# Kernel tuning notes

Measured on AMD Instinct MI355X. Metric: run time of the kernel, lower is better.

Reference implementation:

```python
import jax, jax.numpy as jnp
import numpy as np

N, C, H = 4096, 1024, 16
HD = C // H            # 64
DR = HD // 8           # 8 rope freqs per spatial axis


def setup_inputs() -> dict:
    key = jax.random.key(0)
    k1, k2, k3, k4, k5, k6 = jax.random.split(key, 6)
    x = jax.random.normal(k1, (N, C), dtype=jnp.float32)
    coords = jax.random.randint(k2, (N, 5), 0, 64, dtype=jnp.int32)  # [batch, t, h, w, z]
    w_qkv = jax.random.normal(k3, (3 * C, C), dtype=jnp.float32) / np.sqrt(C)
    w_out = jax.random.normal(k4, (C, C), dtype=jnp.float32) / np.sqrt(C)
    gamma_q = jnp.ones((H, HD), dtype=jnp.float32)
    gamma_k = jnp.ones((H, HD), dtype=jnp.float32)
    return {"x": x, "coords": coords, "w_qkv": w_qkv, "w_out": w_out,
            "gamma_q": gamma_q, "gamma_k": gamma_k}


def _rms_norm(t, gamma):
    # F.normalize(dim=-1) * gamma * sqrt(head_dim), computed in fp32
    t = t.astype(jnp.float32)
    nrm = jnp.linalg.norm(t, axis=-1, keepdims=True)
    return t / jnp.maximum(nrm, 1e-12) * gamma * np.float32(np.sqrt(HD))


def _rope_angles(coords):
    # freqs = 1/10000^(arange(DR)/HD); angles per axis (t,h,w,z), concat -> [N, 4*DR] = [N, HD/2]
    freqs = 1.0 / (10000.0 ** (jnp.arange(DR, dtype=jnp.float32) / HD))
    pos = coords[:, 1:].astype(jnp.float32)  # [N,4]
    ang = pos[:, :, None] * freqs[None, None, :]  # [N,4,DR]
    return ang.reshape(ang.shape[0], -1)  # [N, HD/2]


def _apply_rope(t, cos, sin):
    # t: [N,H,HD]; pairs (2i, 2i+1) rotated by angle[i]
    t2 = t.astype(jnp.float32).reshape(t.shape[0], t.shape[1], -1, 2)
    re = t2[..., 0] * cos - t2[..., 1] * sin
    im = t2[..., 0] * sin + t2[..., 1] * cos
    return jnp.stack([re, im], axis=-1).reshape(t.shape)


def reference(x, coords, w_qkv, w_out, gamma_q, gamma_k):
    n = x.shape[0]
    qkv = (x @ w_qkv.T).reshape(n, 3, H, HD)
    q, k, v = qkv[:, 0], qkv[:, 1], qkv[:, 2]  # [N,H,HD]
    q = _rms_norm(q, gamma_q)
    k = _rms_norm(k, gamma_k)
    ang = _rope_angles(coords)              # [N, HD/2]
    cos = jnp.cos(ang)[:, None, :]          # [N,1,HD/2] (broadcast over heads)
    sin = jnp.sin(ang)[:, None, :]
    q = _apply_rope(q, cos, sin)
    k = _apply_rope(k, cos, sin)
    scale = np.float32(1.0 / np.sqrt(HD))
    scores = jnp.einsum('nhd,mhd->hnm', q, k) * scale  # [H,N,N]
    attn = jax.nn.softmax(scores, axis=-1)
    out = jnp.einsum('hnm,mhd->nhd', attn, v).reshape(n, C)
    return out @ w_out.T
```

## Files before the change

kernel.cpp:

```cpp
#include <hip/hip_runtime.h>
#include <hip/hip_bf16.h>

typedef _Float16 half8 __attribute__((ext_vector_type(8)));
typedef _Float16 half4v __attribute__((ext_vector_type(4)));
typedef _Float16 half2 __attribute__((ext_vector_type(2)));
typedef float f32x4 __attribute__((ext_vector_type(4)));

constexpr int NT = 4096;
constexpr int CH = 1024;
constexpr int NH = 16;
constexpr int HD = 64;
constexpr int C3 = 3072;

#if __has_builtin(__builtin_amdgcn_exp2f)
#define EXP2(x) __builtin_amdgcn_exp2f(x)
#else
#define EXP2(x) exp2f(x)
#endif

#define GLOAD_LDS16(gp, lp) __builtin_amdgcn_global_load_lds( \
    (const __attribute__((address_space(1))) void*)(gp),      \
    (__attribute__((address_space(3))) void*)(lp), 16, 0, 0)

static __device__ inline half2 pk_f16(float a, float b) {
  auto r = __builtin_amdgcn_cvt_pkrtz(a, b);
  return *(half2*)&r;
}

__global__ __launch_bounds__(256) void cvt_kernel(const float* __restrict__ in,
                                                  _Float16* __restrict__ out, int n4) {
  int i = blockIdx.x * 256 + threadIdx.x;
  if (i >= n4) return;
  float4 v = ((const float4*)in)[i];
  half4v h;
  h[0] = (_Float16)v.x; h[1] = (_Float16)v.y; h[2] = (_Float16)v.z; h[3] = (_Float16)v.w;
  ((half4v*)out)[i] = h;
}

template <typename OutT>
__global__ __launch_bounds__(256) void gemm_bt(const _Float16* __restrict__ A,
                                               const _Float16* __restrict__ Bt,
                                               OutT* __restrict__ Cc,
                                               int M, int Nn, int K) {
  __shared__ _Float16 As[128][32];
  __shared__ _Float16 Bs[128][32];
  const int tid = threadIdx.x;
  const int lane = tid & 63, w = tid >> 6;
  const int l15 = lane & 15, l4 = lane >> 4;
  const int m0 = blockIdx.x * 128, n0 = blockIdx.y * 128;
  const int wr = w >> 1, wc = w & 1;
  const int rb = w * 32;
  const int rl = lane >> 2;
  const int cb = (lane & 3) * 8;
  f32x4 acc[4][4] = {};
  for (int k0 = 0; k0 < K; k0 += 32) {
    __syncthreads();
    GLOAD_LDS16(A  + (size_t)(m0 + rb + rl) * K + k0 + cb,      &As[rb][0]);
    GLOAD_LDS16(A  + (size_t)(m0 + rb + 16 + rl) * K + k0 + cb, &As[rb + 16][0]);
    GLOAD_LDS16(Bt + (size_t)(n0 + rb + rl) * K + k0 + cb,      &Bs[rb][0]);
    GLOAD_LDS16(Bt + (size_t)(n0 + rb + 16 + rl) * K + k0 + cb, &Bs[rb + 16][0]);
    __syncthreads();
    half8 af[4], bf[4];
#pragma unroll
    for (int mt = 0; mt < 4; ++mt) af[mt] = *(half8*)&As[wr * 64 + mt * 16 + l15][l4 * 8];
#pragma unroll
    for (int nt = 0; nt < 4; ++nt) bf[nt] = *(half8*)&Bs[wc * 64 + nt * 16 + l15][l4 * 8];
#pragma unroll
    for (int mt = 0; mt < 4; ++mt)
#pragma unroll
      for (int nt = 0; nt < 4; ++nt)
        acc[mt][nt] = __builtin_amdgcn_mfma_f32_16x16x32_f16(af[mt], bf[nt], acc[mt][nt], 0, 0, 0);
  }
#pragma unroll
  for (int mt = 0; mt < 4; ++mt)
#pragma unroll
    for (int nt = 0; nt < 4; ++nt)
#pragma unroll
      for (int r = 0; r < 4; ++r) {
        int row = m0 + wr * 64 + mt * 16 + l4 * 4 + r;
        int col = n0 + wc * 64 + nt * 16 + l15;
        Cc[(size_t)row * Nn + col] = (OutT)acc[mt][nt][r];
      }
}

__global__ __launch_bounds__(256) void rmsrope_kernel(const _Float16* __restrict__ qkv,
                                                      const int* __restrict__ coords,
                                                      const float* __restrict__ gq,
                                                      const float* __restrict__ gk,
                                                      _Float16* __restrict__ Qh,
                                                      _Float16* __restrict__ KF) {
  int gw = blockIdx.x * 4 + (threadIdx.x >> 6);
  int lane = threadIdx.x & 63;
  int n = gw >> 4, h = gw & 15;
  float q = (float)qkv[(size_t)n * C3 + h * HD + lane];
  float k = (float)qkv[(size_t)n * C3 + CH + h * HD + lane];
  float sq = q * q, sk = k * k;
#pragma unroll
  for (int m = 1; m < 64; m <<= 1) { sq += __shfl_xor(sq, m); sk += __shfl_xor(sk, m); }
  q *= 8.0f / fmaxf(sqrtf(sq), 1e-12f) * gq[h * HD + lane];
  k *= 8.0f / fmaxf(sqrtf(sk), 1e-12f) * gk[h * HD + lane];
  int j = lane >> 1, p = j >> 3, dr = j & 7;
  float ang = (float)coords[n * 5 + 1 + p] * __expf(-(float)dr * 0.14391157f);
  float cs = cosf(ang), sn = sinf(ang);
  float qp = __shfl_xor(q, 1), kp = __shfl_xor(k, 1);
  float qr, kr;
  if ((lane & 1) == 0) { qr = q * cs - qp * sn; kr = k * cs - kp * sn; }
  else                 { qr = qp * sn + q * cs; kr = kp * sn + k * cs; }
  Qh[((size_t)h * NT + n) * HD + lane] = (_Float16)(qr * 0.18033688f);
  int m64 = n & 63, kb = n >> 6;
  int t   = 2 * (m64 >> 5) + ((m64 >> 2) & 1);
  int i15 = 4 * ((m64 >> 3) & 3) + (m64 & 3);
  int kk = lane >> 5, ll4 = (lane >> 3) & 3, jj = lane & 7;
  KF[(size_t)h * NT * HD + (size_t)kb * 4096 +
     (size_t)(((t * 2 + kk) * 64 + ll4 * 16 + i15) * 8 + jj)] = (_Float16)kr;
}

__global__ __launch_bounds__(256) void vtrans_kernel(const _Float16* __restrict__ qkv,
                                                     _Float16* __restrict__ VF) {
  __shared__ _Float16 L[64][72];
  int h = blockIdx.y, n0 = blockIdx.x * 64, kb = blockIdx.x, t0 = threadIdx.x;
#pragma unroll
  for (int i = 0; i < 2; ++i) {
    int cid = t0 + i * 256, r = cid >> 3, c = cid & 7;
    *(half8*)&L[r][c * 8] = *(const half8*)(qkv + (size_t)(n0 + r) * C3 + 2 * CH + h * HD + c * 8);
  }
  __syncthreads();
#pragma unroll
  for (int i = 0; i < 2; ++i) {
    int cid = t0 + i * 256, d = cid >> 3, c = cid & 7;
    half8 v;
#pragma unroll
    for (int jj = 0; jj < 8; ++jj) v[jj] = L[c * 8 + jj][d];
    size_t flat = (size_t)h * NT * HD + (size_t)kb * 4096 +
                  (size_t)((((d >> 4) * 2 + (c >> 2)) * 64 + (c & 3) * 16 + (d & 15)) * 8);
    *(half8*)(VF + flat) = v;
  }
}

__global__ __launch_bounds__(256, 2) void attn_kernel(const _Float16* __restrict__ Qh,
                                                      const _Float16* __restrict__ KF,
                                                      const _Float16* __restrict__ VF,
                                                      _Float16* __restrict__ Oh) {
  __shared__ _Float16 KB[4096];
  __shared__ _Float16 VB[4096];
  const int tid = threadIdx.x, lane = tid & 63, w = tid >> 6;
  const int l15 = lane & 15, l4 = lane >> 4;
  int bid = blockIdx.x;
  int s = bid >> 3;
  int h = (bid & 7) * 2 + (s >> 5);
  int n0 = (s & 31) * 128;
  half8 qf[2][2];
#pragma unroll
  for (int qb = 0; qb < 2; ++qb)
#pragma unroll
    for (int kk = 0; kk < 2; ++kk)
      qf[qb][kk] = *(const half8*)(Qh + ((size_t)h * NT + n0 + w * 32 + qb * 16 + l15) * HD + kk * 32 + l4 * 8);
  f32x4 acc[2][4] = {};
  f32x4 acc5[2] = {};
  half8 of1 = {};
  if (l15 == 0) {
#pragma unroll
    for (int jq = 0; jq < 8; ++jq) of1[jq] = (_Float16)1.0f;
  }
  const _Float16* KFh = KF + (size_t)h * NT * HD + w * 512 + lane * 8;
  const _Float16* VFh = VF + (size_t)h * NT * HD + w * 512 + lane * 8;
  union U { half8 v; half2 p[4]; };
  for (int kb = 0; kb < 64; ++kb) {
    __syncthreads();
    {
      size_t g0 = (size_t)kb * 4096;
      GLOAD_LDS16(KFh + g0,        &KB[w * 512]);
      GLOAD_LDS16(KFh + g0 + 2048, &KB[2048 + w * 512]);
      GLOAD_LDS16(VFh + g0,        &VB[w * 512]);
      GLOAD_LDS16(VFh + g0 + 2048, &VB[2048 + w * 512]);
    }
    __syncthreads();
    f32x4 sv[2][4] = {};
    __builtin_amdgcn_s_setprio(1);
#pragma unroll
    for (int t = 0; t < 4; ++t)
#pragma unroll
      for (int kk = 0; kk < 2; ++kk) {
        half8 kf = *(half8*)&KB[(t * 2 + kk) * 512 + lane * 8];
        sv[0][t] = __builtin_amdgcn_mfma_f32_16x16x32_f16(kf, qf[0][kk], sv[0][t], 0, 0, 0);
        sv[1][t] = __builtin_amdgcn_mfma_f32_16x16x32_f16(kf, qf[1][kk], sv[1][t], 0, 0, 0);
      }
    __builtin_amdgcn_s_setprio(0);
    U u[2][2];
#pragma unroll
    for (int qb = 0; qb < 2; ++qb) {
      float e[4][4];
#pragma unroll
      for (int t = 0; t < 4; ++t)
#pragma unroll
        for (int r = 0; r < 4; ++r) e[t][r] = EXP2(sv[qb][t][r]);
      u[qb][0].p[0] = pk_f16(e[0][0], e[0][1]); u[qb][0].p[1] = pk_f16(e[0][2], e[0][3]);
      u[qb][0].p[2] = pk_f16(e[1][0], e[1][1]); u[qb][0].p[3] = pk_f16(e[1][2], e[1][3]);
      u[qb][1].p[0] = pk_f16(e[2][0], e[2][1]); u[qb][1].p[1] = pk_f16(e[2][2], e[2][3]);
      u[qb][1].p[2] = pk_f16(e[3][0], e[3][1]); u[qb][1].p[3] = pk_f16(e[3][2], e[3][3]);
    }
    __builtin_amdgcn_s_setprio(1);
#pragma unroll
    for (int t = 0; t < 4; ++t)
#pragma unroll
      for (int kk = 0; kk < 2; ++kk) {
        half8 vf = *(half8*)&VB[(t * 2 + kk) * 512 + lane * 8];
        acc[0][t] = __builtin_amdgcn_mfma_f32_16x16x32_f16(u[0][kk].v, vf, acc[0][t], 0, 0, 0);
        acc[1][t] = __builtin_amdgcn_mfma_f32_16x16x32_f16(u[1][kk].v, vf, acc[1][t], 0, 0, 0);
      }
    acc5[0] = __builtin_amdgcn_mfma_f32_16x16x32_f16(u[0][0].v, of1, acc5[0], 0, 0, 0);
    acc5[0] = __builtin_amdgcn_mfma_f32_16x16x32_f16(u[0][1].v, of1, acc5[0], 0, 0, 0);
    acc5[1] = __builtin_amdgcn_mfma_f32_16x16x32_f16(u[1][0].v, of1, acc5[1], 0, 0, 0);
    acc5[1] = __builtin_amdgcn_mfma_f32_16x16x32_f16(u[1][1].v, of1, acc5[1], 0, 0, 0);
    __builtin_amdgcn_s_setprio(0);
  }
#pragma unroll
  for (int qb = 0; qb < 2; ++qb) {
    float linv[4];
#pragma unroll
    for (int r = 0; r < 4; ++r) linv[r] = 1.0f / __shfl(acc5[qb][r], lane & 48);
#pragma unroll
    for (int t = 0; t < 4; ++t)
#pragma unroll
      for (int r = 0; r < 4; ++r) {
        int row = n0 + w * 32 + qb * 16 + l4 * 4 + r;
        Oh[(size_t)row * CH + h * HD + t * 16 + l15] = (_Float16)(acc[qb][t][r] * linv[r]);
      }
  }
}

extern "C" void kernel_launch(void* const* d_in, const int* in_sizes, int n_in,
                              void* d_out, int out_size, void* d_ws, size_t ws_size,
                              hipStream_t stream) {
  const float* x      = (const float*)d_in[0];
  const int*   coords = (const int*)d_in[1];
  const float* w_qkv  = (const float*)d_in[2];
  const float* w_out  = (const float*)d_in[3];
  const float* gq     = (const float*)d_in[4];
  const float* gk     = (const float*)d_in[5];
  float* out = (float*)d_out;

  char* ws = (char*)d_ws;
  size_t off = 0;
  auto alloc = [&](size_t bytes) { char* p = ws + off; off += bytes; return p; };
  _Float16* xh   = (_Float16*)alloc((size_t)NT * CH * 2);
  _Float16* wqh  = (_Float16*)alloc((size_t)C3 * CH * 2);
  _Float16* woh  = (_Float16*)alloc((size_t)CH * CH * 2);
  _Float16* qkvh = (_Float16*)alloc((size_t)NT * C3 * 2);
  _Float16* Qh   = (_Float16*)alloc((size_t)NT * CH * 2);
  _Float16* KFh  = (_Float16*)alloc((size_t)NT * CH * 2);
  _Float16* VFh  = (_Float16*)alloc((size_t)NT * CH * 2);
  _Float16* Oh   = (_Float16*)alloc((size_t)NT * CH * 2);
  if (off > ws_size) return;

  cvt_kernel<<<NT * CH / 4 / 256, 256, 0, stream>>>(x, xh, NT * CH / 4);
  cvt_kernel<<<C3 * CH / 4 / 256, 256, 0, stream>>>(w_qkv, wqh, C3 * CH / 4);
  cvt_kernel<<<CH * CH / 4 / 256, 256, 0, stream>>>(w_out, woh, CH * CH / 4);
  gemm_bt<_Float16><<<dim3(NT / 128, C3 / 128), 256, 0, stream>>>(xh, wqh, qkvh, NT, C3, CH);
  rmsrope_kernel<<<NT * NH / 4, 256, 0, stream>>>(qkvh, coords, gq, gk, Qh, KFh);
  vtrans_kernel<<<dim3(NT / 64, NH), 256, 0, stream>>>(qkvh, VFh);
  attn_kernel<<<NH * (NT / 128), 256, 0, stream>>>(Qh, KFh, VFh, Oh);
  gemm_bt<float><<<dim3(NT / 128, CH / 128), 256, 0, stream>>>(Oh, woh, out, NT, CH, CH);
}
```

Measured before the change: 178.9 us.

## Double-buffer LDS tiles in GEMM and attention kernels to overlap loads

Both the GEMM and the attention kernel now use two LDS buffers, issuing the global-to-LDS load for the next tile before computing on the current one. This cuts the number of barriers per tile from two to one and lets memory latency hide behind MFMA work. LDS use doubles (attention goes to 32 KB per block), which could limit occupancy. Correctness relies on the compiler inserting vmcnt waits before the barrier for the async LDS loads.

New measurement: 177.6 us. About the same (-0.7%).

```diff
diff --git a/kernel.cpp b/kernel.cpp
--- a/kernel.cpp
+++ b/kernel.cpp
@@ -42,8 +42,8 @@
                                                const _Float16* __restrict__ Bt,
                                                OutT* __restrict__ Cc,
                                                int M, int Nn, int K) {
-  __shared__ _Float16 As[128][32];
-  __shared__ _Float16 Bs[128][32];
+  __shared__ _Float16 As[2][128][32];
+  __shared__ _Float16 Bs[2][128][32];
   const int tid = threadIdx.x;
   const int lane = tid & 63, w = tid >> 6;
   const int l15 = lane & 15, l4 = lane >> 4;
@@ -53,23 +53,33 @@
   const int rl = lane >> 2;
   const int cb = (lane & 3) * 8;
   f32x4 acc[4][4] = {};
-  for (int k0 = 0; k0 < K; k0 += 32) {
-    __syncthreads();
-    GLOAD_LDS16(A  + (size_t)(m0 + rb + rl) * K + k0 + cb,      &As[rb][0]);
-    GLOAD_LDS16(A  + (size_t)(m0 + rb + 16 + rl) * K + k0 + cb, &As[rb + 16][0]);
-    GLOAD_LDS16(Bt + (size_t)(n0 + rb + rl) * K + k0 + cb,      &Bs[rb][0]);
-    GLOAD_LDS16(Bt + (size_t)(n0 + rb + 16 + rl) * K + k0 + cb, &Bs[rb + 16][0]);
-    __syncthreads();
+  auto stage = [&](int k0, int buf) {
+    GLOAD_LDS16(A  + (size_t)(m0 + rb + rl) * K + k0 + cb,      &As[buf][rb][0]);
+    GLOAD_LDS16(A  + (size_t)(m0 + rb + 16 + rl) * K + k0 + cb, &As[buf][rb + 16][0]);
+    GLOAD_LDS16(Bt + (size_t)(n0 + rb + rl) * K + k0 + cb,      &Bs[buf][rb][0]);
+    GLOAD_LDS16(Bt + (size_t)(n0 + rb + 16 + rl) * K + k0 + cb, &Bs[buf][rb + 16][0]);
+  };
+  auto compute = [&](int buf) {
     half8 af[4], bf[4];
 #pragma unroll
-    for (int mt = 0; mt < 4; ++mt) af[mt] = *(half8*)&As[wr * 64 + mt * 16 + l15][l4 * 8];
-#pragma unroll
-    for (int nt = 0; nt < 4; ++nt) bf[nt] = *(half8*)&Bs[wc * 64 + nt * 16 + l15][l4 * 8];
+    for (int mt = 0; mt < 4; ++mt) af[mt] = *(half8*)&As[buf][wr * 64 + mt * 16 + l15][l4 * 8];
+#pragma unroll
+    for (int nt = 0; nt < 4; ++nt) bf[nt] = *(half8*)&Bs[buf][wc * 64 + nt * 16 + l15][l4 * 8];
 #pragma unroll
     for (int mt = 0; mt < 4; ++mt)
 #pragma unroll
       for (int nt = 0; nt < 4; ++nt)
         acc[mt][nt] = __builtin_amdgcn_mfma_f32_16x16x32_f16(af[mt], bf[nt], acc[mt][nt], 0, 0, 0);
+  };
+  stage(0, 0);
+  __syncthreads();
+  for (int k0 = 0; k0 < K; k0 += 64) {
+    stage(k0 + 32, 1);
+    compute(0);
+    __syncthreads();
+    if (k0 + 64 < K) stage(k0 + 64, 0);
+    compute(1);
+    __syncthreads();
   }
 #pragma unroll
   for (int mt = 0; mt < 4; ++mt)
@@ -141,8 +151,8 @@
                                                       const _Float16* __restrict__ KF,
                                                       const _Float16* __restrict__ VF,
                                                       _Float16* __restrict__ Oh) {
-  __shared__ _Float16 KB[4096];
-  __shared__ _Float16 VB[4096];
+  __shared__ _Float16 KB[2][4096];
+  __shared__ _Float16 VB[2][4096];
   const int tid = threadIdx.x, lane = tid & 63, w = tid >> 6;
   const int l15 = lane & 15, l4 = lane >> 4;
   int bid = blockIdx.x;
@@ -165,23 +175,21 @@
   const _Float16* KFh = KF + (size_t)h * NT * HD + w * 512 + lane * 8;
   const _Float16* VFh = VF + (size_t)h * NT * HD + w * 512 + lane * 8;
   union U { half8 v; half2 p[4]; };
-  for (int kb = 0; kb < 64; ++kb) {
-    __syncthreads();
-    {
-      size_t g0 = (size_t)kb * 4096;
-      GLOAD_LDS16(KFh + g0,        &KB[w * 512]);
-      GLOAD_LDS16(KFh + g0 + 2048, &KB[2048 + w * 512]);
-      GLOAD_LDS16(VFh + g0,        &VB[w * 512]);
-      GLOAD_LDS16(VFh + g0 + 2048, &VB[2048 + w * 512]);
-    }
-    __syncthreads();
+  auto stage = [&](int kb, int buf) {
+    size_t g0 = (size_t)kb * 4096;
+    GLOAD_LDS16(KFh + g0,        &KB[buf][w * 512]);
+    GLOAD_LDS16(KFh + g0 + 2048, &KB[buf][2048 + w * 512]);
+    GLOAD_LDS16(VFh + g0,        &VB[buf][w * 512]);
+    GLOAD_LDS16(VFh + g0 + 2048, &VB[buf][2048 + w * 512]);
+  };
+  auto compute = [&](int buf) {
     f32x4 sv[2][4] = {};
     __builtin_amdgcn_s_setprio(1);
 #pragma unroll
     for (int t = 0; t < 4; ++t)
 #pragma unroll
       for (int kk = 0; kk < 2; ++kk) {
-        half8 kf = *(half8*)&KB[(t * 2 + kk) * 512 + lane * 8];
+        half8 kf = *(half8*)&KB[buf][(t * 2 + kk) * 512 + lane * 8];
         sv[0][t] = __builtin_amdgcn_mfma_f32_16x16x32_f16(kf, qf[0][kk], sv[0][t], 0, 0, 0);
         sv[1][t] = __builtin_amdgcn_mfma_f32_16x16x32_f16(kf, qf[1][kk], sv[1][t], 0, 0, 0);
       }
@@ -204,7 +212,7 @@
     for (int t = 0; t < 4; ++t)
 #pragma unroll
       for (int kk = 0; kk < 2; ++kk) {
-        half8 vf = *(half8*)&VB[(t * 2 + kk) * 512 + lane * 8];
+        half8 vf = *(half8*)&VB[buf][(t * 2 + kk) * 512 + lane * 8];
         acc[0][t] = __builtin_amdgcn_mfma_f32_16x16x32_f16(u[0][kk].v, vf, acc[0][t], 0, 0, 0);
         acc[1][t] = __builtin_amdgcn_mfma_f32_16x16x32_f16(u[1][kk].v, vf, acc[1][t], 0, 0, 0);
       }
@@ -213,6 +221,16 @@
     acc5[1] = __builtin_amdgcn_mfma_f32_16x16x32_f16(u[1][0].v, of1, acc5[1], 0, 0, 0);
     acc5[1] = __builtin_amdgcn_mfma_f32_16x16x32_f16(u[1][1].v, of1, acc5[1], 0, 0, 0);
     __builtin_amdgcn_s_setprio(0);
+  };
+  stage(0, 0);
+  __syncthreads();
+  for (int kb = 0; kb < 64; kb += 2) {
+    stage(kb + 1, 1);
+    compute(0);
+    __syncthreads();
+    if (kb + 2 < 64) stage(kb + 2, 0);
+    compute(1);
+    __syncthreads();
   }
 #pragma unroll
   for (int qb = 0; qb < 2; ++qb) {
```
